# Kernel optimization log

Hardware: AMD Instinct MI355X
Metric: run time of the kernel (lower is better)

## Reference

```python
import jax, jax.numpy as jnp
import numpy as np

B, P, H, W, K = 2, 4096, 128, 128, 8
RADIUS = 0.05  # NDC-space point radius (raster_settings.radius)


def setup_inputs() -> dict:
    key = jax.random.key(0)
    k1, k2, k3 = jax.random.split(key, 3)
    points_world = jax.random.normal(k1, (B, P, 3), jnp.float32)
    # near-identity rotation (row-vector convention: X_view = X_world @ R + T)
    R = jnp.eye(3, dtype=jnp.float32)[None] + 0.01 * jax.random.normal(k2, (B, 3, 3), jnp.float32)
    # translate cloud to z ~ +3 so points are in front of the camera
    T = (0.1 * jax.random.normal(k3, (B, 3), jnp.float32)).at[:, 2].add(3.0)
    focal = jnp.full((B,), 1.5, jnp.float32)
    return {"points_world": points_world, "R": R, "T": T, "focal": focal}


def reference(points_world, R, T, focal):
    # --- camera transform: world -> view -> NDC (z kept in view space) ---
    pts_view = jnp.einsum('bpi,bij->bpj', points_world, R) + T[:, None, :]  # [B,P,3]
    z = pts_view[..., 2]                                                    # [B,P]
    x_ndc = focal[:, None] * pts_view[..., 0] / z
    y_ndc = focal[:, None] * pts_view[..., 1] / z

    # --- pixel-center NDC grid (pytorch3d convention: +x left, +y up) ---
    gx = 1.0 - 2.0 * (jnp.arange(W, dtype=jnp.float32) + 0.5) / W  # [W]
    gy = 1.0 - 2.0 * (jnp.arange(H, dtype=jnp.float32) + 0.5) / H  # [H]
    GY, GX = jnp.meshgrid(gy, gx, indexing='ij')
    gxf = GX.reshape(-1)  # [HW]
    gyf = GY.reshape(-1)

    # --- per-pixel candidate search: squared NDC distance to every point ---
    dist2 = (gxf[None, :, None] - x_ndc[:, None, :]) ** 2 \
          + (gyf[None, :, None] - y_ndc[:, None, :]) ** 2      # [B,HW,P]
    inside = (dist2 < RADIUS * RADIUS) & (z[:, None, :] > 0.0)  # in radius & in front

    # --- depth-sorted top-K nearest-in-z among covering points ---
    keyz = jnp.where(inside, z[:, None, :], jnp.inf)            # [B,HW,P]
    neg_top, idx_top = jax.lax.top_k(-keyz, K)                  # K smallest z
    zk = jnp.take_along_axis(keyz, idx_top, axis=-1)            # [B,HW,K]
    dk = jnp.take_along_axis(dist2, idx_top, axis=-1)
    valid = jnp.isfinite(zk)

    idx = jnp.where(valid, idx_top, -1).reshape(B, H, W, K)
    zbuf = jnp.where(valid, zk, -1.0).reshape(B, H, W, K)
    dists = jnp.where(valid, dk, -1.0).reshape(B, H, W, K)
    return idx, zbuf, dists
```

## Files before the change

kernel.cpp:

```cpp
#include <hip/hip_runtime.h>
#include <math.h>

#define BB 2
#define PP 4096
#define HH 128
#define WW 128
#define KK 8
#define TS 8
#define NTX (WW / TS)
#define NTY (HH / TS)
#define NW 4
#define SEG (PP / NW)

typedef float vfloat4 __attribute__((ext_vector_type(4)));

__global__ __launch_bounds__(64 * NW, 2) void raster_kernel(
    const float* __restrict__ pw,
    const float* __restrict__ Rm,
    const float* __restrict__ Tv,
    const float* __restrict__ fo,
    float* __restrict__ out,
    int N)
{
    __shared__ float4 cand[NW][SEG];

    const int tx = blockIdx.x, ty = blockIdx.y, b = blockIdx.z;
    const int wv   = threadIdx.x >> 6;
    const int lane = threadIdx.x & 63;

    const float* r = Rm + b * 9;
    const float r00=r[0], r01=r[1], r02=r[2];
    const float r10=r[3], r11=r[4], r12=r[5];
    const float r20=r[6], r21=r[7], r22=r[8];
    const float t0=Tv[b*3+0], t1=Tv[b*3+1], t2=Tv[b*3+2];
    const float f = fo[b];

    const float R2f   = (float)(0.05 * 0.05);
    const float apron = 0.05f + 1e-5f;

    float gx_hi = 1.0f - 2.0f * ((float)(tx * TS)          + 0.5f) / (float)WW;
    float gx_lo = 1.0f - 2.0f * ((float)(tx * TS + TS - 1) + 0.5f) / (float)WW;
    float gy_hi = 1.0f - 2.0f * ((float)(ty * TS)          + 0.5f) / (float)HH;
    float gy_lo = 1.0f - 2.0f * ((float)(ty * TS + TS - 1) + 0.5f) / (float)HH;
    const float xmin = gx_lo - apron, xmax = gx_hi + apron;
    const float ymin = gy_lo - apron, ymax = gy_hi + apron;

    int cnt = 0;
    const float* pwb = pw + (size_t)b * PP * 3;
    const float* qp = pwb + (wv * SEG + lane) * 3;
    float cx = qp[0], cy = qp[1], cz = qp[2];
    for (int it = 0; it < SEG / 64; ++it) {
        float nx = 0.f, ny = 0.f, nz = 0.f;
        if (it + 1 < SEG / 64) {
            const float* qn = qp + (it + 1) * 192;
            nx = qn[0]; ny = qn[1]; nz = qn[2];
        }
        int i = wv * SEG + it * 64 + lane;
        float x = cx, y = cy, z = cz;
        float vx = __fadd_rn(__fadd_rn(__fadd_rn(__fmul_rn(x, r00), __fmul_rn(y, r10)), __fmul_rn(z, r20)), t0);
        float vy = __fadd_rn(__fadd_rn(__fadd_rn(__fmul_rn(x, r01), __fmul_rn(y, r11)), __fmul_rn(z, r21)), t1);
        float vz = __fadd_rn(__fadd_rn(__fadd_rn(__fmul_rn(x, r02), __fmul_rn(y, r12)), __fmul_rn(z, r22)), t2);
        float xn = __fmul_rn(f, vx) / vz;
        float yn = __fmul_rn(f, vy) / vz;
        bool keep = (vz > 0.0f) && (xn >= xmin) && (xn <= xmax)
                                && (yn >= ymin) && (yn <= ymax);
        unsigned long long m = __ballot(keep);
        if (keep) {
            int pos = __popcll(m & ((1ull << lane) - 1ull));
            cand[wv][cnt + pos] = make_float4(xn, yn, vz, __int_as_float(i));
        }
        cnt += __popcll(m);
        cx = nx; cy = ny; cz = nz;
    }

    int w = tx * TS + (lane & (TS - 1));
    int h = ty * TS + (lane / TS);
    float gx = 1.0f - 2.0f * ((float)w + 0.5f) / (float)WW;
    float gy = 1.0f - 2.0f * ((float)h + 0.5f) / (float)HH;

    float zk[KK], dk[KK]; int ik[KK];
#pragma unroll
    for (int j = 0; j < KK; ++j) { zk[j] = INFINITY; dk[j] = -1.0f; ik[j] = -1; }

    for (int s = 0; s < cnt; ++s) {
        float4 q = cand[wv][s];
        float dx = __fsub_rn(gx, q.x);
        float dy = __fsub_rn(gy, q.y);
        float d2 = __fadd_rn(__fmul_rn(dx, dx), __fmul_rn(dy, dy));
        float z = q.z;
        if (d2 < R2f && z < zk[KK - 1]) {
            int i = __float_as_int(q.w);
#pragma unroll
            for (int j = KK - 1; j >= 1; --j) {
                if (z < zk[j]) {
                    if (z < zk[j - 1]) { zk[j] = zk[j-1]; ik[j] = ik[j-1]; dk[j] = dk[j-1]; }
                    else               { zk[j] = z;       ik[j] = i;       dk[j] = d2;      }
                }
            }
            if (z < zk[0]) { zk[0] = z; ik[0] = i; dk[0] = d2; }
        }
    }

    __syncthreads();
    float* mz = (float*)&cand[0][0];
    float* mi = mz + NW * KK * 64;
    float* md = mi + NW * KK * 64;
#pragma unroll
    for (int s = 0; s < KK; ++s) {
        mz[(wv * KK + s) * 64 + lane] = zk[s];
        mi[(wv * KK + s) * 64 + lane] = __int_as_float(ik[s]);
        md[(wv * KK + s) * 64 + lane] = dk[s];
    }
    __syncthreads();

    if (wv == 0) {
        float hz[NW], hd[NW]; int hi_[NW], hp[NW];
#pragma unroll
        for (int wq = 0; wq < NW; ++wq) {
            hp[wq]  = 0;
            hz[wq]  = mz[(wq * KK) * 64 + lane];
            hi_[wq] = __float_as_int(mi[(wq * KK) * 64 + lane]);
            hd[wq]  = md[(wq * KK) * 64 + lane];
        }
        float A[KK], Z[KK], D[KK];
#pragma unroll
        for (int o = 0; o < KK; ++o) {
            int bw = 0;
#pragma unroll
            for (int wq = 1; wq < NW; ++wq) {
                bool better = (hz[wq] < hz[bw]) ||
                              ((hz[wq] == hz[bw]) && (hi_[wq] < hi_[bw]));
                if (better) bw = wq;
            }
            float sz = hz[0], sd = hd[0]; int si = hi_[0];
#pragma unroll
            for (int wq = 1; wq < NW; ++wq) {
                if (bw == wq) { sz = hz[wq]; sd = hd[wq]; si = hi_[wq]; }
            }
            A[o] = (float)si;
            Z[o] = (si >= 0) ? sz : -1.0f;
            D[o] = sd;
#pragma unroll
            for (int wq = 0; wq < NW; ++wq) {
                if (bw == wq) {
                    int p = ++hp[wq];
                    if (p < KK) {
                        hz[wq]  = mz[(wq * KK + p) * 64 + lane];
                        hi_[wq] = __float_as_int(mi[(wq * KK + p) * 64 + lane]);
                        hd[wq]  = md[(wq * KK + p) * 64 + lane];
                    } else {
                        hz[wq] = INFINITY; hi_[wq] = -1; hd[wq] = -1.0f;
                    }
                }
            }
        }
        int pix  = (b * HH + h) * WW + w;
        int base = pix * KK;
        vfloat4* oa = (vfloat4*)(out + base);
        vfloat4* oz = (vfloat4*)(out + N + base);
        vfloat4* od = (vfloat4*)(out + 2 * N + base);
        __builtin_nontemporal_store(((vfloat4*)A)[0], oa);
        __builtin_nontemporal_store(((vfloat4*)A)[1], oa + 1);
        __builtin_nontemporal_store(((vfloat4*)Z)[0], oz);
        __builtin_nontemporal_store(((vfloat4*)Z)[1], oz + 1);
        __builtin_nontemporal_store(((vfloat4*)D)[0], od);
        __builtin_nontemporal_store(((vfloat4*)D)[1], od + 1);
    }
}

extern "C" void kernel_launch(void* const* d_in, const int* in_sizes, int n_in,
                              void* d_out, int out_size, void* d_ws, size_t ws_size,
                              hipStream_t stream) {
    const float* pw = (const float*)d_in[0];
    const float* Rm = (const float*)d_in[1];
    const float* Tv = (const float*)d_in[2];
    const float* fo = (const float*)d_in[3];
    int N = out_size / 3;

    hipLaunchKernelGGL(raster_kernel, dim3(NTX, NTY, BB), dim3(64 * NW), 0, stream,
                       pw, Rm, Tv, fo, (float*)d_out, N);
}
```

Baseline: 85.63 us.

## Precompute point projection in separate kernel instead of per tile

Adds a small project_kernel that transforms every point to NDC once and writes float4 (x, y, z) into workspace memory. The raster kernel then loads these precomputed points with fully unrolled vector loads instead of redoing the rotation, translation and two divisions for every point in every tile. This removes the repeated projection work done by each of the 512 blocks, but adds a second kernel launch and a global-memory round trip through the workspace.

```diff
diff --git a/kernel.cpp b/kernel.cpp
--- a/kernel.cpp
+++ b/kernel.cpp
@@ -11,14 +11,34 @@
 #define NTY (HH / TS)
 #define NW 4
 #define SEG (PP / NW)
+#define CIT (SEG / 64)
 
 typedef float vfloat4 __attribute__((ext_vector_type(4)));
 
-__global__ __launch_bounds__(64 * NW, 2) void raster_kernel(
+__global__ __launch_bounds__(256) void project_kernel(
     const float* __restrict__ pw,
     const float* __restrict__ Rm,
     const float* __restrict__ Tv,
     const float* __restrict__ fo,
+    float4* __restrict__ pts)
+{
+    int t = blockIdx.x * blockDim.x + threadIdx.x;
+    if (t >= BB * PP) return;
+    int b = t >> 12;
+    const float* r = Rm + b * 9;
+    const float* q = pw + (size_t)t * 3;
+    float x = q[0], y = q[1], z = q[2];
+    float vx = __fadd_rn(__fadd_rn(__fadd_rn(__fmul_rn(x, r[0]), __fmul_rn(y, r[3])), __fmul_rn(z, r[6])), Tv[b*3+0]);
+    float vy = __fadd_rn(__fadd_rn(__fadd_rn(__fmul_rn(x, r[1]), __fmul_rn(y, r[4])), __fmul_rn(z, r[7])), Tv[b*3+1]);
+    float vz = __fadd_rn(__fadd_rn(__fadd_rn(__fmul_rn(x, r[2]), __fmul_rn(y, r[5])), __fmul_rn(z, r[8])), Tv[b*3+2]);
+    float f = fo[b];
+    float xn = __fmul_rn(f, vx) / vz;
+    float yn = __fmul_rn(f, vy) / vz;
+    pts[t] = make_float4(xn, yn, vz, 0.0f);
+}
+
+__global__ __launch_bounds__(64 * NW, 2) void raster_kernel(
+    const float4* __restrict__ pts,
     float* __restrict__ out,
     int N)
 {
@@ -27,13 +47,6 @@
     const int tx = blockIdx.x, ty = blockIdx.y, b = blockIdx.z;
     const int wv   = threadIdx.x >> 6;
     const int lane = threadIdx.x & 63;
-
-    const float* r = Rm + b * 9;
-    const float r00=r[0], r01=r[1], r02=r[2];
-    const float r10=r[3], r11=r[4], r12=r[5];
-    const float r20=r[6], r21=r[7], r22=r[8];
-    const float t0=Tv[b*3+0], t1=Tv[b*3+1], t2=Tv[b*3+2];
-    const float f = fo[b];
 
     const float R2f   = (float)(0.05 * 0.05);
     const float apron = 0.05f + 1e-5f;
@@ -45,32 +58,24 @@
     const float xmin = gx_lo - apron, xmax = gx_hi + apron;
     const float ymin = gy_lo - apron, ymax = gy_hi + apron;
 
+    const float4* pb = pts + (size_t)b * PP + wv * SEG + lane;
+    float4 pf[CIT];
+#pragma unroll
+    for (int it = 0; it < CIT; ++it) pf[it] = pb[it * 64];
+
     int cnt = 0;
-    const float* pwb = pw + (size_t)b * PP * 3;
-    const float* qp = pwb + (wv * SEG + lane) * 3;
-    float cx = qp[0], cy = qp[1], cz = qp[2];
-    for (int it = 0; it < SEG / 64; ++it) {
-        float nx = 0.f, ny = 0.f, nz = 0.f;
-        if (it + 1 < SEG / 64) {
-            const float* qn = qp + (it + 1) * 192;
-            nx = qn[0]; ny = qn[1]; nz = qn[2];
-        }
+#pragma unroll
+    for (int it = 0; it < CIT; ++it) {
+        float4 q = pf[it];
         int i = wv * SEG + it * 64 + lane;
-        float x = cx, y = cy, z = cz;
-        float vx = __fadd_rn(__fadd_rn(__fadd_rn(__fmul_rn(x, r00), __fmul_rn(y, r10)), __fmul_rn(z, r20)), t0);
-        float vy = __fadd_rn(__fadd_rn(__fadd_rn(__fmul_rn(x, r01), __fmul_rn(y, r11)), __fmul_rn(z, r21)), t1);
-        float vz = __fadd_rn(__fadd_rn(__fadd_rn(__fmul_rn(x, r02), __fmul_rn(y, r12)), __fmul_rn(z, r22)), t2);
-        float xn = __fmul_rn(f, vx) / vz;
-        float yn = __fmul_rn(f, vy) / vz;
-        bool keep = (vz > 0.0f) && (xn >= xmin) && (xn <= xmax)
-                                && (yn >= ymin) && (yn <= ymax);
+        bool keep = (q.z > 0.0f) && (q.x >= xmin) && (q.x <= xmax)
+                                 && (q.y >= ymin) && (q.y <= ymax);
         unsigned long long m = __ballot(keep);
         if (keep) {
             int pos = __popcll(m & ((1ull << lane) - 1ull));
-            cand[wv][cnt + pos] = make_float4(xn, yn, vz, __int_as_float(i));
+            cand[wv][cnt + pos] = make_float4(q.x, q.y, q.z, __int_as_float(i));
         }
         cnt += __popcll(m);
-        cx = nx; cy = ny; cz = nz;
     }
 
     int w = tx * TS + (lane & (TS - 1));
@@ -177,6 +182,10 @@
     const float* fo = (const float*)d_in[3];
     int N = out_size / 3;
 
+    float4* pts = (float4*)d_ws;
+
+    hipLaunchKernelGGL(project_kernel, dim3((BB * PP + 255) / 256), dim3(256), 0, stream,
+                       pw, Rm, Tv, fo, pts);
     hipLaunchKernelGGL(raster_kernel, dim3(NTX, NTY, BB), dim3(64 * NW), 0, stream,
-                       pw, Rm, Tv, fo, (float*)d_out, N);
+                       pts, (float*)d_out, N);
 }
```

After: 85.81 us. No clear change (+0.2%).
